# Kernel optimization log

Hardware: AMD Instinct MI355X
Metric: run time of the kernel (lower is better)

## Reference

```python
import jax, jax.numpy as jnp
import numpy as np

# column-index constants for the node feature matrix and edge attributes
VM, VA, PG, QG, PD, QD = 0, 1, 2, 3, 4, 5
G_COL, B_COL = 0, 1

N_NODES = 100000
N_EDGES = 3200000
N_FEAT = 6


def setup_inputs() -> dict:
    key = jax.random.key(0)
    k1, k2, k3, k4, k5, k6 = jax.random.split(key, 6)
    pred = jax.random.normal(k1, (N_NODES, N_FEAT), dtype=jnp.float32)
    target = jax.random.normal(k2, (N_NODES, N_FEAT), dtype=jnp.float32)
    src = jax.random.randint(k3, (N_EDGES,), 0, N_NODES, dtype=jnp.int32)
    dst = jax.random.randint(k4, (N_EDGES,), 0, N_NODES, dtype=jnp.int32)
    edge_index = jnp.stack([src, dst], axis=0)
    edge_attr = jax.random.normal(k5, (N_EDGES, 2), dtype=jnp.float32)
    mask = jax.random.bernoulli(k6, 0.5, (N_NODES, N_FEAT))
    return {"pred": pred, "target": target, "edge_index": edge_index,
            "edge_attr": edge_attr, "mask": mask}


def reference(pred, target, edge_index, edge_attr, mask):
    # temp_pred[~mask] = target[~mask]
    tp = jnp.where(mask, pred, target)

    V_m = tp[:, VM]
    V_a = tp[:, VA]
    V = V_m * jnp.exp(1j * V_a)           # complex64 [N]
    V_conj = jnp.conj(V)

    # conj(Y_bus) entries on edges: G - jB
    Y_conj = edge_attr[:, G_COL] - 1j * edge_attr[:, B_COL]  # complex64 [E]

    row, col = edge_index[0], edge_index[1]
    # (Y_bus_conj @ V_conj)[i] = sum over edges (i,j) of conj(Y_ij) * conj(V_j)
    msg = Y_conj * V_conj[col]                               # gather-multiply [E]
    matvec = jax.ops.segment_sum(msg, row, num_segments=tp.shape[0])  # scatter-add [N]

    S_injection = V * matvec                                  # diag(V) @ (...)

    net_P = tp[:, PG] - tp[:, PD]
    net_Q = tp[:, QG] - tp[:, QD]
    diff = (net_P + 1j * net_Q) - S_injection

    loss = jnp.mean(jnp.abs(diff))
    real_loss = jnp.mean(jnp.abs(jnp.real(diff)))
    imag_loss = jnp.mean(jnp.abs(jnp.imag(diff)))
    return (loss, real_loss, imag_loss)
```

## Files before the change

kernel.cpp:

```cpp
#include <hip/hip_runtime.h>
#include <math.h>

constexpr int N_NODES = 100000;
constexpr int N_EDGES = 3200000;
constexpr int NF      = 6;

constexpr int BSHIFT  = 10;
constexpr int BNODES  = 1 << BSHIFT;
constexpr int NB      = (N_NODES + BNODES - 1) >> BSHIFT;
constexpr int CAP     = 36864;
constexpr int NSLICE  = 8;
constexpr int TILE    = 2048;
constexpr int EPT     = TILE / 256;
constexpr int NBLK_PART = (N_EDGES + TILE - 1) / TILE;

constexpr size_t OFF_V    = 0;
constexpr size_t OFF_MSG  = OFF_V + (size_t)N_NODES * 8;
constexpr size_t OFF_LROW = OFF_MSG + (size_t)NB * CAP * 8;
constexpr size_t OFF_PART = OFF_LROW + (size_t)NB * CAP * 2;
constexpr size_t OFF_CNT  = OFF_PART + (size_t)NB * NSLICE * BNODES * 8;
constexpr size_t OFF_SUMS = OFF_CNT + 400;
constexpr size_t WS_NEED  = OFF_CNT + 512;

__global__ void node_prep(const float* __restrict__ pred,
                          const float* __restrict__ target,
                          const unsigned char* __restrict__ mask,
                          float2* __restrict__ v) {
    int i = blockIdx.x * blockDim.x + threadIdx.x;
    if (i >= N_NODES) return;
    const int b = i * NF;
    float vm = mask[b + 0] ? pred[b + 0] : target[b + 0];
    float va = mask[b + 1] ? pred[b + 1] : target[b + 1];
    float s, c;
    sincosf(va, &s, &c);
    v[i] = make_float2(vm * c, vm * s);
}

__global__ __launch_bounds__(256) void partition_edges(
        const int* __restrict__ row, const int* __restrict__ col,
        const float2* __restrict__ attr, const float2* __restrict__ v,
        unsigned int* __restrict__ gcur,
        unsigned short* __restrict__ lrow_g, float2* __restrict__ msg_g) {
    __shared__ unsigned int h[4][NB];
    __shared__ unsigned int cur[4][NB];
    __shared__ int wb[4][NB];
    __shared__ int dbase[NB];
    __shared__ unsigned int tot_s[NB];
    __shared__ unsigned int rr_s[TILE];
    __shared__ float2 msg_s[TILE];
    __shared__ int total_s;

    const int tid = threadIdx.x;
    const int w = tid >> 6;
    const int e0 = blockIdx.x * TILE;

    for (int i = tid; i < 4 * NB; i += 256) {
        (&h[0][0])[i] = 0u;
        (&cur[0][0])[i] = 0u;
    }
    __syncthreads();

    int r[EPT];
    #pragma unroll
    for (int k = 0; k < EPT; ++k) {
        int e = e0 + k * 256 + tid;
        if (e < N_EDGES) {
            r[k] = row[e];
            atomicAdd(&h[w][r[k] >> BSHIFT], 1u);
        } else {
            r[k] = -1;
        }
    }
    __syncthreads();

    if (tid < NB)
        tot_s[tid] = h[0][tid] + h[1][tid] + h[2][tid] + h[3][tid];
    __syncthreads();

    if (tid < NB) {
        int lbase = 0;
        for (int j = 0; j < tid; ++j) lbase += (int)tot_s[j];
        unsigned t0 = h[0][tid], t1 = h[1][tid], t2 = h[2][tid];
        unsigned tot = tot_s[tid];
        unsigned g = tot ? atomicAdd(&gcur[tid], tot) : 0u;
        dbase[tid] = (int)g - lbase;
        wb[0][tid] = lbase;
        wb[1][tid] = lbase + (int)t0;
        wb[2][tid] = lbase + (int)(t0 + t1);
        wb[3][tid] = lbase + (int)(t0 + t1 + t2);
        if (tid == NB - 1) total_s = lbase + (int)tot;
    }
    __syncthreads();

    #pragma unroll
    for (int k = 0; k < EPT; ++k) {
        int rr = r[k];
        if (rr < 0) continue;
        int e = e0 + k * 256 + tid;
        int b = rr >> BSHIFT;
        int slot = wb[w][b] + (int)atomicAdd(&cur[w][b], 1u);
        int c = col[e];
        float2 gb = attr[e];
        float2 vv = v[c];
        float mre = fmaf(gb.x, vv.x, -gb.y * vv.y);
        float mim = -fmaf(gb.x, vv.y, gb.y * vv.x);
        rr_s[slot] = (unsigned)rr;
        msg_s[slot] = make_float2(mre, mim);
    }
    __syncthreads();

    const int total = total_s;
    for (int j = tid; j < total; j += 256) {
        unsigned rr = rr_s[j];
        int b = (int)(rr >> BSHIFT);
        int g = dbase[b] + j;
        if (g < CAP) {
            size_t idx = (size_t)b * CAP + g;
            msg_g[idx] = msg_s[j];
            lrow_g[idx] = (unsigned short)(rr & (BNODES - 1));
        }
    }
}

__global__ __launch_bounds__(256) void bucket_accum(
        const unsigned int* __restrict__ gcur,
        const unsigned short* __restrict__ lrow,
        const float2* __restrict__ msg,
        float2* __restrict__ partials) {
    __shared__ float acc[BNODES][2];
    const int b = blockIdx.x / NSLICE;
    const int s = blockIdx.x % NSLICE;
    int cnt = (int)min(gcur[b], (unsigned)CAP);
    for (int i = threadIdx.x; i < BNODES; i += 256) { acc[i][0] = 0.f; acc[i][1] = 0.f; }
    __syncthreads();
    int per = (cnt + NSLICE - 1) / NSLICE;
    int st = s * per;
    int en = min(st + per, cnt);
    const unsigned short* lr = lrow + (size_t)b * CAP;
    const float2* m = msg + (size_t)b * CAP;
    for (int j = st + threadIdx.x; j < en; j += 256) {
        int li = lr[j];
        float2 mm = m[j];
        atomicAdd(&acc[li][0], mm.x);
        atomicAdd(&acc[li][1], mm.y);
    }
    __syncthreads();
    float2* p = partials + (size_t)blockIdx.x * BNODES;
    for (int i = threadIdx.x; i < BNODES; i += 256)
        p[i] = make_float2(acc[i][0], acc[i][1]);
}

__global__ void finalize_nodes(const float* __restrict__ pred,
                               const float* __restrict__ target,
                               const unsigned char* __restrict__ mask,
                               const float2* __restrict__ v,
                               const float2* __restrict__ partials,
                               float* __restrict__ sums) {
    int i = blockIdx.x * blockDim.x + threadIdx.x;
    float a = 0.f, ar = 0.f, ai = 0.f;
    if (i < N_NODES) {
        const int bb = i >> BSHIFT;
        const int li = i & (BNODES - 1);
        float mr = 0.f, mi = 0.f;
        #pragma unroll
        for (int s = 0; s < NSLICE; ++s) {
            float2 p = partials[((size_t)(bb * NSLICE + s)) * BNODES + li];
            mr += p.x; mi += p.y;
        }
        const int b = i * NF;
        float pg = mask[b + 2] ? pred[b + 2] : target[b + 2];
        float qg = mask[b + 3] ? pred[b + 3] : target[b + 3];
        float pd = mask[b + 4] ? pred[b + 4] : target[b + 4];
        float qd = mask[b + 5] ? pred[b + 5] : target[b + 5];
        float netP = pg - pd;
        float netQ = qg - qd;
        float2 vv = v[i];
        float s_re = vv.x * mr - vv.y * mi;
        float s_im = vv.x * mi + vv.y * mr;
        float dre = netP - s_re;
        float dim = netQ - s_im;
        ar = fabsf(dre);
        ai = fabsf(dim);
        a  = sqrtf(dre * dre + dim * dim);
    }
    #pragma unroll
    for (int off = 32; off > 0; off >>= 1) {
        a  += __shfl_down(a,  off, 64);
        ar += __shfl_down(ar, off, 64);
        ai += __shfl_down(ai, off, 64);
    }
    __shared__ float red[3][4];
    int wave = threadIdx.x >> 6;
    int lane = threadIdx.x & 63;
    if (lane == 0) { red[0][wave] = a; red[1][wave] = ar; red[2][wave] = ai; }
    __syncthreads();
    if (threadIdx.x == 0) {
        atomicAdd(&sums[0], red[0][0] + red[0][1] + red[0][2] + red[0][3]);
        atomicAdd(&sums[1], red[1][0] + red[1][1] + red[1][2] + red[1][3]);
        atomicAdd(&sums[2], red[2][0] + red[2][1] + red[2][2] + red[2][3]);
    }
}

__global__ void write_out(const float* __restrict__ sums, float* __restrict__ out) {
    if (threadIdx.x == 0 && blockIdx.x == 0) {
        const float inv = 1.0f / (float)N_NODES;
        out[0] = sums[0] * inv;
        out[1] = sums[1] * inv;
        out[2] = sums[2] * inv;
    }
}

__global__ void edge_scatter_fb(const int* __restrict__ row,
                                const int* __restrict__ col,
                                const float2* __restrict__ attr,
                                const float2* __restrict__ v,
                                float2* __restrict__ mv) {
    int e = blockIdx.x * blockDim.x + threadIdx.x;
    if (e >= N_EDGES) return;
    int r = row[e];
    int c = col[e];
    float2 gb = attr[e];
    float2 vv = v[c];
    float mre = fmaf(gb.x, vv.x, -gb.y * vv.y);
    float mim = -fmaf(gb.x, vv.y, gb.y * vv.x);
    atomicAdd(&mv[r].x, mre);
    atomicAdd(&mv[r].y, mim);
}

__global__ void finalize_fb(const float* __restrict__ pred,
                            const float* __restrict__ target,
                            const unsigned char* __restrict__ mask,
                            const float2* __restrict__ v,
                            const float2* __restrict__ mv,
                            float* __restrict__ sums) {
    int i = blockIdx.x * blockDim.x + threadIdx.x;
    float a = 0.f, ar = 0.f, ai = 0.f;
    if (i < N_NODES) {
        const int b = i * NF;
        float pg = mask[b + 2] ? pred[b + 2] : target[b + 2];
        float qg = mask[b + 3] ? pred[b + 3] : target[b + 3];
        float pd = mask[b + 4] ? pred[b + 4] : target[b + 4];
        float qd = mask[b + 5] ? pred[b + 5] : target[b + 5];
        float netP = pg - pd;
        float netQ = qg - qd;
        float2 vv = v[i];
        float2 m = mv[i];
        float s_re = vv.x * m.x - vv.y * m.y;
        float s_im = vv.x * m.y + vv.y * m.x;
        float dre = netP - s_re;
        float dim = netQ - s_im;
        ar = fabsf(dre);
        ai = fabsf(dim);
        a  = sqrtf(dre * dre + dim * dim);
    }
    #pragma unroll
    for (int off = 32; off > 0; off >>= 1) {
        a  += __shfl_down(a,  off, 64);
        ar += __shfl_down(ar, off, 64);
        ai += __shfl_down(ai, off, 64);
    }
    __shared__ float red[3][4];
    int wave = threadIdx.x >> 6;
    int lane = threadIdx.x & 63;
    if (lane == 0) { red[0][wave] = a; red[1][wave] = ar; red[2][wave] = ai; }
    __syncthreads();
    if (threadIdx.x == 0) {
        atomicAdd(&sums[0], red[0][0] + red[0][1] + red[0][2] + red[0][3]);
        atomicAdd(&sums[1], red[1][0] + red[1][1] + red[1][2] + red[1][3]);
        atomicAdd(&sums[2], red[2][0] + red[2][1] + red[2][2] + red[2][3]);
    }
}

extern "C" void kernel_launch(void* const* d_in, const int* in_sizes, int n_in,
                              void* d_out, int out_size, void* d_ws, size_t ws_size,
                              hipStream_t stream) {
    const float*         pred   = (const float*)d_in[0];
    const float*         target = (const float*)d_in[1];
    const int*           eidx   = (const int*)d_in[2];
    const float2*        attr   = (const float2*)d_in[3];
    const unsigned char* mask   = (const unsigned char*)d_in[4];
    float* out = (float*)d_out;

    const int* row = eidx;
    const int* col = eidx + N_EDGES;

    char* ws = (char*)d_ws;
    const int B = 256;

    if (ws_size >= WS_NEED) {
        float2*         v        = (float2*)(ws + OFF_V);
        float2*         msg      = (float2*)(ws + OFF_MSG);
        unsigned short* lrow     = (unsigned short*)(ws + OFF_LROW);
        float2*         partials = (float2*)(ws + OFF_PART);
        unsigned int*   gcur     = (unsigned int*)(ws + OFF_CNT);
        float*          sums     = (float*)(ws + OFF_SUMS);

        hipMemsetAsync(ws + OFF_CNT, 0, 512, stream);
        node_prep<<<(N_NODES + B - 1) / B, B, 0, stream>>>(pred, target, mask, v);
        partition_edges<<<NBLK_PART, B, 0, stream>>>(row, col, attr, v, gcur, lrow, msg);
        bucket_accum<<<NB * NSLICE, B, 0, stream>>>(gcur, lrow, msg, partials);
        finalize_nodes<<<(N_NODES + B - 1) / B, B, 0, stream>>>(pred, target, mask, v,
                                                                partials, sums);
        write_out<<<1, 64, 0, stream>>>(sums, out);
    } else {
        float2* v    = (float2*)ws;
        float2* mv   = (float2*)(ws + (size_t)N_NODES * 8);
        float*  sums = (float*)(ws + 2ull * N_NODES * 8);
        hipMemsetAsync(mv, 0, (size_t)N_NODES * 8 + 16, stream);
        node_prep<<<(N_NODES + B - 1) / B, B, 0, stream>>>(pred, target, mask, v);
        edge_scatter_fb<<<(N_EDGES + B - 1) / B, B, 0, stream>>>(row, col, attr, v, mv);
        finalize_fb<<<(N_NODES + B - 1) / B, B, 0, stream>>>(pred, target, mask, v, mv, sums);
        write_out<<<1, 64, 0, stream>>>(sums, out);
    }
}
```

Before: 220.9 us.

## Fuse bucket accumulation, node finalize and output via last-block completion counters

Merges the per-bucket shared-memory accumulation, the per-node loss finalize and the output write into one kernel. The last slice block to finish a bucket does that bucket's finalize, and the last bucket writes the means. Counter zeroing moves into node_prep, which removes the memset launch, and the number of slices per bucket drops from 8 to 4. This saves several launches and a pass over the partials, at the cost of fewer blocks in the accumulation and serialized tail work on the last blocks.

```diff
diff --git a/kernel.cpp b/kernel.cpp
--- a/kernel.cpp
+++ b/kernel.cpp
@@ -9,7 +9,7 @@
 constexpr int BNODES  = 1 << BSHIFT;
 constexpr int NB      = (N_NODES + BNODES - 1) >> BSHIFT;
 constexpr int CAP     = 36864;
-constexpr int NSLICE  = 8;
+constexpr int NSLICE  = 4;
 constexpr int TILE    = 2048;
 constexpr int EPT     = TILE / 256;
 constexpr int NBLK_PART = (N_EDGES + TILE - 1) / TILE;
@@ -19,14 +19,16 @@
 constexpr size_t OFF_LROW = OFF_MSG + (size_t)NB * CAP * 8;
 constexpr size_t OFF_PART = OFF_LROW + (size_t)NB * CAP * 2;
 constexpr size_t OFF_CNT  = OFF_PART + (size_t)NB * NSLICE * BNODES * 8;
-constexpr size_t OFF_SUMS = OFF_CNT + 400;
-constexpr size_t WS_NEED  = OFF_CNT + 512;
+constexpr int    CTR_WORDS = 1024 / 4;
+constexpr size_t WS_NEED  = OFF_CNT + 1024;
 
 __global__ void node_prep(const float* __restrict__ pred,
                           const float* __restrict__ target,
                           const unsigned char* __restrict__ mask,
-                          float2* __restrict__ v) {
+                          float2* __restrict__ v,
+                          unsigned int* __restrict__ ctr) {
     int i = blockIdx.x * blockDim.x + threadIdx.x;
+    if (blockIdx.x == 0 && threadIdx.x < CTR_WORDS) ctr[threadIdx.x] = 0u;
     if (i >= N_NODES) return;
     const int b = i * NF;
     float vm = mask[b + 0] ? pred[b + 0] : target[b + 0];
@@ -122,56 +124,66 @@
     }
 }
 
-__global__ __launch_bounds__(256) void bucket_accum(
+__global__ __launch_bounds__(256) void accum_finalize(
         const unsigned int* __restrict__ gcur,
         const unsigned short* __restrict__ lrow,
         const float2* __restrict__ msg,
-        float2* __restrict__ partials) {
-    __shared__ float acc[BNODES][2];
+        float2* __restrict__ partials,
+        unsigned int* __restrict__ sdone,
+        float* __restrict__ sums,
+        unsigned int* __restrict__ done_all,
+        const float* __restrict__ pred,
+        const float* __restrict__ target,
+        const unsigned char* __restrict__ mask,
+        const float2* __restrict__ v,
+        float* __restrict__ out) {
+    __shared__ float acc_re[BNODES];
+    __shared__ float acc_im[BNODES];
+    __shared__ unsigned int old_s;
+    const int tid = threadIdx.x;
     const int b = blockIdx.x / NSLICE;
     const int s = blockIdx.x % NSLICE;
     int cnt = (int)min(gcur[b], (unsigned)CAP);
-    for (int i = threadIdx.x; i < BNODES; i += 256) { acc[i][0] = 0.f; acc[i][1] = 0.f; }
+    for (int i = tid; i < BNODES; i += 256) { acc_re[i] = 0.f; acc_im[i] = 0.f; }
     __syncthreads();
     int per = (cnt + NSLICE - 1) / NSLICE;
     int st = s * per;
     int en = min(st + per, cnt);
     const unsigned short* lr = lrow + (size_t)b * CAP;
     const float2* m = msg + (size_t)b * CAP;
-    for (int j = st + threadIdx.x; j < en; j += 256) {
+    for (int j = st + tid; j < en; j += 256) {
         int li = lr[j];
         float2 mm = m[j];
-        atomicAdd(&acc[li][0], mm.x);
-        atomicAdd(&acc[li][1], mm.y);
-    }
-    __syncthreads();
-    float2* p = partials + (size_t)blockIdx.x * BNODES;
-    for (int i = threadIdx.x; i < BNODES; i += 256)
-        p[i] = make_float2(acc[i][0], acc[i][1]);
-}
-
-__global__ void finalize_nodes(const float* __restrict__ pred,
-                               const float* __restrict__ target,
-                               const unsigned char* __restrict__ mask,
-                               const float2* __restrict__ v,
-                               const float2* __restrict__ partials,
-                               float* __restrict__ sums) {
-    int i = blockIdx.x * blockDim.x + threadIdx.x;
+        atomicAdd(&acc_re[li], mm.x);
+        atomicAdd(&acc_im[li], mm.y);
+    }
+    __syncthreads();
+    float2* p = partials + ((size_t)b * NSLICE + s) * BNODES;
+    for (int i = tid; i < BNODES; i += 256)
+        p[i] = make_float2(acc_re[i], acc_im[i]);
+
+    __threadfence();
+    __syncthreads();
+    if (tid == 0) old_s = atomicAdd(&sdone[b], 1u);
+    __syncthreads();
+    if (old_s != (unsigned)(NSLICE - 1)) return;
+    __threadfence();
+
     float a = 0.f, ar = 0.f, ai = 0.f;
-    if (i < N_NODES) {
-        const int bb = i >> BSHIFT;
-        const int li = i & (BNODES - 1);
+    for (int li = tid; li < BNODES; li += 256) {
+        int i = (b << BSHIFT) + li;
+        if (i >= N_NODES) break;
         float mr = 0.f, mi = 0.f;
         #pragma unroll
-        for (int s = 0; s < NSLICE; ++s) {
-            float2 p = partials[((size_t)(bb * NSLICE + s)) * BNODES + li];
-            mr += p.x; mi += p.y;
+        for (int s2 = 0; s2 < NSLICE; ++s2) {
+            float2 pp = partials[((size_t)b * NSLICE + s2) * BNODES + li];
+            mr += pp.x; mi += pp.y;
         }
-        const int b = i * NF;
-        float pg = mask[b + 2] ? pred[b + 2] : target[b + 2];
-        float qg = mask[b + 3] ? pred[b + 3] : target[b + 3];
-        float pd = mask[b + 4] ? pred[b + 4] : target[b + 4];
-        float qd = mask[b + 5] ? pred[b + 5] : target[b + 5];
+        const int bb = i * NF;
+        float pg = mask[bb + 2] ? pred[bb + 2] : target[bb + 2];
+        float qg = mask[bb + 3] ? pred[bb + 3] : target[bb + 3];
+        float pd = mask[bb + 4] ? pred[bb + 4] : target[bb + 4];
+        float qd = mask[bb + 5] ? pred[bb + 5] : target[bb + 5];
         float netP = pg - pd;
         float netQ = qg - qd;
         float2 vv = v[i];
@@ -179,9 +191,9 @@
         float s_im = vv.x * mi + vv.y * mr;
         float dre = netP - s_re;
         float dim = netQ - s_im;
-        ar = fabsf(dre);
-        ai = fabsf(dim);
-        a  = sqrtf(dre * dre + dim * dim);
+        ar += fabsf(dre);
+        ai += fabsf(dim);
+        a  += sqrtf(dre * dre + dim * dim);
     }
     #pragma unroll
     for (int off = 32; off > 0; off >>= 1) {
@@ -190,23 +202,22 @@
         ai += __shfl_down(ai, off, 64);
     }
     __shared__ float red[3][4];
-    int wave = threadIdx.x >> 6;
-    int lane = threadIdx.x & 63;
+    int wave = tid >> 6;
+    int lane = tid & 63;
     if (lane == 0) { red[0][wave] = a; red[1][wave] = ar; red[2][wave] = ai; }
     __syncthreads();
-    if (threadIdx.x == 0) {
+    if (tid == 0) {
         atomicAdd(&sums[0], red[0][0] + red[0][1] + red[0][2] + red[0][3]);
         atomicAdd(&sums[1], red[1][0] + red[1][1] + red[1][2] + red[1][3]);
         atomicAdd(&sums[2], red[2][0] + red[2][1] + red[2][2] + red[2][3]);
-    }
-}
-
-__global__ void write_out(const float* __restrict__ sums, float* __restrict__ out) {
-    if (threadIdx.x == 0 && blockIdx.x == 0) {
-        const float inv = 1.0f / (float)N_NODES;
-        out[0] = sums[0] * inv;
-        out[1] = sums[1] * inv;
-        out[2] = sums[2] * inv;
+        __threadfence();
+        unsigned fin = atomicAdd(done_all, 1u);
+        if (fin == (unsigned)(NB - 1)) {
+            const float inv = 1.0f / (float)N_NODES;
+            out[0] = atomicAdd(&sums[0], 0.f) * inv;
+            out[1] = atomicAdd(&sums[1], 0.f) * inv;
+            out[2] = atomicAdd(&sums[2], 0.f) * inv;
+        }
     }
 }
 
@@ -271,6 +282,15 @@
     }
 }
 
+__global__ void write_out_fb(const float* __restrict__ sums, float* __restrict__ out) {
+    if (threadIdx.x == 0 && blockIdx.x == 0) {
+        const float inv = 1.0f / (float)N_NODES;
+        out[0] = sums[0] * inv;
+        out[1] = sums[1] * inv;
+        out[2] = sums[2] * inv;
+    }
+}
+
 extern "C" void kernel_launch(void* const* d_in, const int* in_sizes, int n_in,
                               void* d_out, int out_size, void* d_ws, size_t ws_size,
                               hipStream_t stream) {
@@ -292,24 +312,26 @@
         float2*         msg      = (float2*)(ws + OFF_MSG);
         unsigned short* lrow     = (unsigned short*)(ws + OFF_LROW);
         float2*         partials = (float2*)(ws + OFF_PART);
+        unsigned int*   ctr      = (unsigned int*)(ws + OFF_CNT);
         unsigned int*   gcur     = (unsigned int*)(ws + OFF_CNT);
-        float*          sums     = (float*)(ws + OFF_SUMS);
-
-        hipMemsetAsync(ws + OFF_CNT, 0, 512, stream);
-        node_prep<<<(N_NODES + B - 1) / B, B, 0, stream>>>(pred, target, mask, v);
+        unsigned int*   sdone    = (unsigned int*)(ws + OFF_CNT + 512);
+        float*          sums     = (float*)(ws + OFF_CNT + 912);
+        unsigned int*   done_all = (unsigned int*)(ws + OFF_CNT + 928);
+
+        node_prep<<<(N_NODES + B - 1) / B, B, 0, stream>>>(pred, target, mask, v, ctr);
         partition_edges<<<NBLK_PART, B, 0, stream>>>(row, col, attr, v, gcur, lrow, msg);
-        bucket_accum<<<NB * NSLICE, B, 0, stream>>>(gcur, lrow, msg, partials);
-        finalize_nodes<<<(N_NODES + B - 1) / B, B, 0, stream>>>(pred, target, mask, v,
-                                                                partials, sums);
-        write_out<<<1, 64, 0, stream>>>(sums, out);
+        accum_finalize<<<NB * NSLICE, B, 0, stream>>>(gcur, lrow, msg, partials,
+                                                      sdone, sums, done_all,
+                                                      pred, target, mask, v, out);
     } else {
         float2* v    = (float2*)ws;
         float2* mv   = (float2*)(ws + (size_t)N_NODES * 8);
         float*  sums = (float*)(ws + 2ull * N_NODES * 8);
         hipMemsetAsync(mv, 0, (size_t)N_NODES * 8 + 16, stream);
-        node_prep<<<(N_NODES + B - 1) / B, B, 0, stream>>>(pred, target, mask, v);
+        unsigned int* dummy = (unsigned int*)(ws + 2ull * N_NODES * 8 + 64);
+        node_prep<<<(N_NODES + B - 1) / B, B, 0, stream>>>(pred, target, mask, v, dummy);
         edge_scatter_fb<<<(N_EDGES + B - 1) / B, B, 0, stream>>>(row, col, attr, v, mv);
         finalize_fb<<<(N_NODES + B - 1) / B, B, 0, stream>>>(pred, target, mask, v, mv, sums);
-        write_out<<<1, 64, 0, stream>>>(sums, out);
-    }
-}
+        write_out_fb<<<1, 64, 0, stream>>>(sums, out);
+    }
+}
```

Measured after the change: 266.3 us. +20.5%, slower.
